# Kernel optimization log

Hardware: AMD Instinct MI355X
Metric: run time of the kernel (lower is better)

Reference implementation:

```python
import jax, jax.numpy as jnp
import numpy as np

ROUTING_ITER = 3
EPS = 1e-8


def squash(caps, axis=-1, eps=EPS):
    dot = jnp.sum(caps * caps, axis=axis, keepdims=True)
    scale = dot / (1.0 + dot) / jnp.sqrt(dot + eps)
    return scale * caps


def setup_inputs() -> dict:
    key = jax.random.key(0)
    k1, k2, k3 = jax.random.split(key, 3)
    B, I, O, D_in, D_out = 32, 1024, 64, 16, 32
    x = jax.random.normal(k1, (B, I, D_in), dtype=jnp.float32)
    W = jax.random.normal(k2, (1, I, O, D_out, D_in), dtype=jnp.float32) * 0.05
    b = jax.random.normal(k3, (1, 1, O, D_out), dtype=jnp.float32) * 0.05
    return {"x": x, "W": W, "b": b}


def reference(x, W, b):
    # u_hat[b,i,o,d] = sum_n W[0,i,o,d,n] * x[b,i,n]
    u_hat = jnp.einsum('iodn,bin->biod', W[0], x)  # [B, I, O, D_out]
    u_hat_det = jax.lax.stop_gradient(u_hat)
    B, I, O, _ = u_hat.shape
    b_ij = jnp.zeros((B, I, O, 1), dtype=x.dtype)
    v_j = None
    for it in range(ROUTING_ITER):
        c_ij = jax.nn.softmax(b_ij, axis=2)  # over output capsules
        if it == ROUTING_ITER - 1:
            s_j = jnp.sum(c_ij * u_hat, axis=1, keepdims=True) + b  # [B,1,O,D]
            v_j = squash(s_j, axis=-1)
        else:
            s_j = jnp.sum(c_ij * u_hat_det, axis=1, keepdims=True)
            v_j = squash(s_j, axis=-1)
            a_ij = jnp.sum(u_hat_det * v_j, axis=-1, keepdims=True)  # agreement
            b_ij = b_ij + a_ij
    return jnp.squeeze(v_j)  # [B, O, D_out]
```

## Files before the change

### kernel.cpp

```cpp
#include <hip/hip_runtime.h>
#include <hip/hip_bf16.h>
#include <stdint.h>

#define B_  32
#define I_  1024
#define O_  64
#define D_  32
#define N_  16
#define OD_ 2048

__device__ __forceinline__ uint32_t f2bf1(float f) {
  uint32_t u = __float_as_uint(f);
  return (u + 0x7fffu + ((u >> 16) & 1u)) >> 16;
}
__device__ __forceinline__ uint32_t pack2(float a, float b) {
  return f2bf1(a) | (f2bf1(b) << 16);
}
__device__ __forceinline__ void unpack8(uint4 r, float u[8]) {
  u[0] = __uint_as_float(r.x << 16);
  u[1] = __uint_as_float(r.x & 0xffff0000u);
  u[2] = __uint_as_float(r.y << 16);
  u[3] = __uint_as_float(r.y & 0xffff0000u);
  u[4] = __uint_as_float(r.z << 16);
  u[5] = __uint_as_float(r.z & 0xffff0000u);
  u[6] = __uint_as_float(r.w << 16);
  u[7] = __uint_as_float(r.w & 0xffff0000u);
}

__global__ __launch_bounds__(256) void k_einsum(const float* __restrict__ x,
                                                const float* __restrict__ W,
                                                uint4* __restrict__ uhat) {
  const int i = blockIdx.x;
  const int t = threadIdx.x;
  __shared__ float xs[B_ * N_];
  for (int e = t; e < B_ * N_; e += 256) {
    int bb = e >> 4, n = e & 15;
    xs[e] = x[(size_t)bb * (I_ * N_) + (size_t)i * N_ + n];
  }
  float w[8][16];
  const float* Wi = W + (size_t)i * (OD_ * N_) + (size_t)t * (8 * N_);
  #pragma unroll
  for (int k = 0; k < 8; ++k) {
    #pragma unroll
    for (int q = 0; q < 4; ++q) {
      float4 f = ((const float4*)(Wi + k * 16))[q];
      w[k][q * 4 + 0] = f.x; w[k][q * 4 + 1] = f.y;
      w[k][q * 4 + 2] = f.z; w[k][q * 4 + 3] = f.w;
    }
  }
  __syncthreads();
  for (int bb = 0; bb < B_; ++bb) {
    float xv[16];
    #pragma unroll
    for (int q = 0; q < 4; ++q) {
      float4 f = ((const float4*)(xs + bb * 16))[q];
      xv[q * 4 + 0] = f.x; xv[q * 4 + 1] = f.y;
      xv[q * 4 + 2] = f.z; xv[q * 4 + 3] = f.w;
    }
    float acc[8];
    #pragma unroll
    for (int k = 0; k < 8; ++k) {
      float a = 0.f;
      #pragma unroll
      for (int n = 0; n < 16; ++n) a = fmaf(w[k][n], xv[n], a);
      acc[k] = a;
    }
    uint4 outv = make_uint4(pack2(acc[0], acc[1]), pack2(acc[2], acc[3]),
                            pack2(acc[4], acc[5]), pack2(acc[6], acc[7]));
    uhat[(((size_t)bb * I_ + i) * OD_ + (size_t)t * 8) >> 3] = outv;
  }
}

__global__ __launch_bounds__(256) void k_sum0(const uint4* __restrict__ uhat,
                                              float* __restrict__ part) {
  const int b = blockIdx.x >> 5, chunk = blockIdx.x & 31;
  const int t = threadIdx.x;
  float acc[8] = {0.f, 0.f, 0.f, 0.f, 0.f, 0.f, 0.f, 0.f};
  for (int ii = 0; ii < 32; ++ii) {
    const int i = chunk * 32 + ii;
    uint4 r = uhat[(((size_t)b * I_ + i) * OD_ + (size_t)t * 8) >> 3];
    float u[8]; unpack8(r, u);
    #pragma unroll
    for (int j = 0; j < 8; ++j) acc[j] += u[j];
  }
  float* o = part + ((size_t)b * 32 + chunk) * OD_ + (size_t)t * 8;
  ((float4*)o)[0] = make_float4(acc[0], acc[1], acc[2], acc[3]);
  ((float4*)o)[1] = make_float4(acc[4], acc[5], acc[6], acc[7]);
}

__global__ __launch_bounds__(256) void k_squash(const float* __restrict__ part,
                                                const float* __restrict__ bias,
                                                float* __restrict__ vout,
                                                float scale, int addBias) {
  const int lane = threadIdx.x & 63;
  const int row = blockIdx.x * 4 + (threadIdx.x >> 6);
  const int b = row >> 6, o = row & 63;
  const int d = lane & 31;
  const float* p = part + (size_t)b * (32 * OD_) + (size_t)o * 32 + d;
  float s = 0.f;
  const int c0 = (lane >> 5) * 16;
  for (int c = c0; c < c0 + 16; ++c) s += p[(size_t)c * OD_];
  s += __shfl_xor(s, 32);
  s *= scale;
  if (addBias) s += bias[o * 32 + d];
  float dot = s * s;
  #pragma unroll
  for (int off = 1; off <= 16; off <<= 1) dot += __shfl_xor(dot, off);
  float sc = dot / (1.f + dot) / sqrtf(dot + 1e-8f);
  if (lane < 32) vout[(size_t)row * 32 + d] = s * sc;
}

__global__ __launch_bounds__(256) void k_route(const uint4* __restrict__ uhat,
                                               const float* __restrict__ vprev,
                                               float* __restrict__ bij,
                                               float* __restrict__ part,
                                               int secondIter) {
  const int b = blockIdx.x >> 5, chunk = blockIdx.x & 31;
  const int t = threadIdx.x;
  __shared__ float abuf[64];
  __shared__ float cbuf[64];
  float vreg[8];
  {
    const float4* vp = (const float4*)(vprev + (size_t)b * OD_ + (size_t)t * 8);
    float4 v0 = vp[0], v1 = vp[1];
    vreg[0] = v0.x; vreg[1] = v0.y; vreg[2] = v0.z; vreg[3] = v0.w;
    vreg[4] = v1.x; vreg[5] = v1.y; vreg[6] = v1.z; vreg[7] = v1.w;
  }
  float s_acc[8] = {0.f, 0.f, 0.f, 0.f, 0.f, 0.f, 0.f, 0.f};
  for (int ii = 0; ii < 32; ++ii) {
    const int i = chunk * 32 + ii;
    uint4 r = uhat[(((size_t)b * I_ + i) * OD_ + (size_t)t * 8) >> 3];
    float u[8]; unpack8(r, u);
    float p = 0.f;
    #pragma unroll
    for (int j = 0; j < 8; ++j) p = fmaf(u[j], vreg[j], p);
    p += __shfl_xor(p, 1);
    p += __shfl_xor(p, 2);
    if ((t & 3) == 0) abuf[t >> 2] = p;
    __syncthreads();
    if (t < 64) {
      float a = abuf[t];
      const size_t bidx = ((size_t)b * I_ + i) * 64 + t;
      float bn;
      if (secondIter) bn = bij[bidx] + a;
      else            { bn = a; bij[bidx] = bn; }
      float m = bn;
      #pragma unroll
      for (int off = 1; off <= 32; off <<= 1) m = fmaxf(m, __shfl_xor(m, off));
      float e = __expf(bn - m);
      float sm = e;
      #pragma unroll
      for (int off = 1; off <= 32; off <<= 1) sm += __shfl_xor(sm, off);
      cbuf[t] = e / sm;
    }
    __syncthreads();
    const float c = cbuf[t >> 2];
    #pragma unroll
    for (int j = 0; j < 8; ++j) s_acc[j] = fmaf(c, u[j], s_acc[j]);
  }
  float* o = part + ((size_t)b * 32 + chunk) * OD_ + (size_t)t * 8;
  ((float4*)o)[0] = make_float4(s_acc[0], s_acc[1], s_acc[2], s_acc[3]);
  ((float4*)o)[1] = make_float4(s_acc[4], s_acc[5], s_acc[6], s_acc[7]);
}

extern "C" void kernel_launch(void* const* d_in, const int* in_sizes, int n_in,
                              void* d_out, int out_size, void* d_ws, size_t ws_size,
                              hipStream_t stream) {
  const float* x    = (const float*)d_in[0];
  const float* W    = (const float*)d_in[1];
  const float* bias = (const float*)d_in[2];
  float* out = (float*)d_out;

  char* ws = (char*)d_ws;
  uint4* uhat = (uint4*)ws;
  float* bij  = (float*)(ws + 134217728ull);
  float* part = (float*)(ws + 134217728ull + 8388608ull);
  float* vbuf = (float*)(ws + 134217728ull + 16777216ull);

  k_einsum<<<dim3(I_), dim3(256), 0, stream>>>(x, W, uhat);
  k_sum0  <<<dim3(1024), dim3(256), 0, stream>>>(uhat, part);
  k_squash<<<dim3(512),  dim3(256), 0, stream>>>(part, bias, vbuf, 1.f / 64.f, 0);
  k_route <<<dim3(1024), dim3(256), 0, stream>>>(uhat, vbuf, bij, part, 0);
  k_squash<<<dim3(512),  dim3(256), 0, stream>>>(part, bias, vbuf, 1.f, 0);
  k_route <<<dim3(1024), dim3(256), 0, stream>>>(uhat, vbuf, bij, part, 1);
  k_squash<<<dim3(512),  dim3(256), 0, stream>>>(part, bias, out, 1.f, 1);
}
```

Measured before the change: 346.1 us.

## Batch routing softmax across 32 inputs and split einsum blocks in half

```diff
diff --git a/kernel.cpp b/kernel.cpp
--- a/kernel.cpp
+++ b/kernel.cpp
@@ -29,18 +29,20 @@
 
 __global__ __launch_bounds__(256) void k_einsum(const float* __restrict__ x,
                                                 const float* __restrict__ W,
-                                                uint4* __restrict__ uhat) {
-  const int i = blockIdx.x;
+                                                uint2* __restrict__ uhat) {
+  const int i = blockIdx.x >> 1;
+  const int half = blockIdx.x & 1;
   const int t = threadIdx.x;
+  const int od_base = half * 1024 + t * 4;
   __shared__ float xs[B_ * N_];
   for (int e = t; e < B_ * N_; e += 256) {
     int bb = e >> 4, n = e & 15;
     xs[e] = x[(size_t)bb * (I_ * N_) + (size_t)i * N_ + n];
   }
-  float w[8][16];
-  const float* Wi = W + (size_t)i * (OD_ * N_) + (size_t)t * (8 * N_);
+  float w[4][16];
+  const float* Wi = W + (size_t)i * (OD_ * N_) + (size_t)od_base * N_;
   #pragma unroll
-  for (int k = 0; k < 8; ++k) {
+  for (int k = 0; k < 4; ++k) {
     #pragma unroll
     for (int q = 0; q < 4; ++q) {
       float4 f = ((const float4*)(Wi + k * 16))[q];
@@ -57,17 +59,16 @@
       xv[q * 4 + 0] = f.x; xv[q * 4 + 1] = f.y;
       xv[q * 4 + 2] = f.z; xv[q * 4 + 3] = f.w;
     }
-    float acc[8];
-    #pragma unroll
-    for (int k = 0; k < 8; ++k) {
+    float acc[4];
+    #pragma unroll
+    for (int k = 0; k < 4; ++k) {
       float a = 0.f;
       #pragma unroll
       for (int n = 0; n < 16; ++n) a = fmaf(w[k][n], xv[n], a);
       acc[k] = a;
     }
-    uint4 outv = make_uint4(pack2(acc[0], acc[1]), pack2(acc[2], acc[3]),
-                            pack2(acc[4], acc[5]), pack2(acc[6], acc[7]));
-    uhat[(((size_t)bb * I_ + i) * OD_ + (size_t)t * 8) >> 3] = outv;
+    uhat[(((size_t)bb * I_ + i) * OD_ + od_base) >> 2] =
+        make_uint2(pack2(acc[0], acc[1]), pack2(acc[2], acc[3]));
   }
 }
 
@@ -110,6 +111,7 @@
   if (lane < 32) vout[(size_t)row * 32 + d] = s * sc;
 }
 
+#define PAD_ 65
 __global__ __launch_bounds__(256) void k_route(const uint4* __restrict__ uhat,
                                                const float* __restrict__ vprev,
                                                float* __restrict__ bij,
@@ -117,8 +119,8 @@
                                                int secondIter) {
   const int b = blockIdx.x >> 5, chunk = blockIdx.x & 31;
   const int t = threadIdx.x;
-  __shared__ float abuf[64];
-  __shared__ float cbuf[64];
+  __shared__ float abuf[32 * PAD_];
+  __shared__ float cbuf[32 * PAD_];
   float vreg[8];
   {
     const float4* vp = (const float4*)(vprev + (size_t)b * OD_ + (size_t)t * 8);
@@ -126,35 +128,64 @@
     vreg[0] = v0.x; vreg[1] = v0.y; vreg[2] = v0.z; vreg[3] = v0.w;
     vreg[4] = v1.x; vreg[5] = v1.y; vreg[6] = v1.z; vreg[7] = v1.w;
   }
-  float s_acc[8] = {0.f, 0.f, 0.f, 0.f, 0.f, 0.f, 0.f, 0.f};
+  const size_t ubase = (((size_t)b * I_ + (size_t)chunk * 32) * OD_ + (size_t)t * 8) >> 3;
   for (int ii = 0; ii < 32; ++ii) {
-    const int i = chunk * 32 + ii;
-    uint4 r = uhat[(((size_t)b * I_ + i) * OD_ + (size_t)t * 8) >> 3];
+    uint4 r = uhat[ubase + (size_t)ii * (OD_ / 8)];
     float u[8]; unpack8(r, u);
     float p = 0.f;
     #pragma unroll
     for (int j = 0; j < 8; ++j) p = fmaf(u[j], vreg[j], p);
     p += __shfl_xor(p, 1);
     p += __shfl_xor(p, 2);
-    if ((t & 3) == 0) abuf[t >> 2] = p;
-    __syncthreads();
-    if (t < 64) {
-      float a = abuf[t];
-      const size_t bidx = ((size_t)b * I_ + i) * 64 + t;
-      float bn;
-      if (secondIter) bn = bij[bidx] + a;
-      else            { bn = a; bij[bidx] = bn; }
-      float m = bn;
+    if ((t & 3) == 0) abuf[ii * PAD_ + (t >> 2)] = p;
+  }
+  __syncthreads();
+  {
+    const int ii = t >> 3;
+    const int ob = (t & 7) * 8;
+    const int i = chunk * 32 + ii;
+    float bn[8];
+    const size_t bidx = ((size_t)b * I_ + i) * 64 + ob;
+    if (secondIter) {
+      float4 b0 = ((const float4*)(bij + bidx))[0];
+      float4 b1 = ((const float4*)(bij + bidx))[1];
+      bn[0] = b0.x + abuf[ii * PAD_ + ob + 0];
+      bn[1] = b0.y + abuf[ii * PAD_ + ob + 1];
+      bn[2] = b0.z + abuf[ii * PAD_ + ob + 2];
+      bn[3] = b0.w + abuf[ii * PAD_ + ob + 3];
+      bn[4] = b1.x + abuf[ii * PAD_ + ob + 4];
+      bn[5] = b1.y + abuf[ii * PAD_ + ob + 5];
+      bn[6] = b1.z + abuf[ii * PAD_ + ob + 6];
+      bn[7] = b1.w + abuf[ii * PAD_ + ob + 7];
+    } else {
       #pragma unroll
-      for (int off = 1; off <= 32; off <<= 1) m = fmaxf(m, __shfl_xor(m, off));
-      float e = __expf(bn - m);
-      float sm = e;
-      #pragma unroll
-      for (int off = 1; off <= 32; off <<= 1) sm += __shfl_xor(sm, off);
-      cbuf[t] = e / sm;
-    }
-    __syncthreads();
-    const float c = cbuf[t >> 2];
+      for (int j = 0; j < 8; ++j) bn[j] = abuf[ii * PAD_ + ob + j];
+      ((float4*)(bij + bidx))[0] = make_float4(bn[0], bn[1], bn[2], bn[3]);
+      ((float4*)(bij + bidx))[1] = make_float4(bn[4], bn[5], bn[6], bn[7]);
+    }
+    float m = bn[0];
+    #pragma unroll
+    for (int j = 1; j < 8; ++j) m = fmaxf(m, bn[j]);
+    m = fmaxf(m, __shfl_xor(m, 1));
+    m = fmaxf(m, __shfl_xor(m, 2));
+    m = fmaxf(m, __shfl_xor(m, 4));
+    float e[8], sm = 0.f;
+    #pragma unroll
+    for (int j = 0; j < 8; ++j) { e[j] = __expf(bn[j] - m); sm += e[j]; }
+    sm += __shfl_xor(sm, 1);
+    sm += __shfl_xor(sm, 2);
+    sm += __shfl_xor(sm, 4);
+    float inv = 1.f / sm;
+    #pragma unroll
+    for (int j = 0; j < 8; ++j) cbuf[ii * PAD_ + ob + j] = e[j] * inv;
+  }
+  __syncthreads();
+  float s_acc[8] = {0.f, 0.f, 0.f, 0.f, 0.f, 0.f, 0.f, 0.f};
+  const int oq = t >> 2;
+  for (int ii = 0; ii < 32; ++ii) {
+    uint4 r = uhat[ubase + (size_t)ii * (OD_ / 8)];
+    float u[8]; unpack8(r, u);
+    const float c = cbuf[ii * PAD_ + oq];
     #pragma unroll
     for (int j = 0; j < 8; ++j) s_acc[j] = fmaf(c, u[j], s_acc[j]);
   }
@@ -172,16 +203,17 @@
   float* out = (float*)d_out;
 
   char* ws = (char*)d_ws;
-  uint4* uhat = (uint4*)ws;
+  uint2* uhat2 = (uint2*)ws;
+  uint4* uhat4 = (uint4*)ws;
   float* bij  = (float*)(ws + 134217728ull);
   float* part = (float*)(ws + 134217728ull + 8388608ull);
   float* vbuf = (float*)(ws + 134217728ull + 16777216ull);
 
-  k_einsum<<<dim3(I_), dim3(256), 0, stream>>>(x, W, uhat);
-  k_sum0  <<<dim3(1024), dim3(256), 0, stream>>>(uhat, part);
+  k_einsum<<<dim3(I_ * 2), dim3(256), 0, stream>>>(x, W, uhat2);
+  k_sum0  <<<dim3(1024), dim3(256), 0, stream>>>(uhat4, part);
   k_squash<<<dim3(512),  dim3(256), 0, stream>>>(part, bias, vbuf, 1.f / 64.f, 0);
-  k_route <<<dim3(1024), dim3(256), 0, stream>>>(uhat, vbuf, bij, part, 0);
+  k_route <<<dim3(1024), dim3(256), 0, stream>>>(uhat4, vbuf, bij, part, 0);
   k_squash<<<dim3(512),  dim3(256), 0, stream>>>(part, bias, vbuf, 1.f, 0);
-  k_route <<<dim3(1024), dim3(256), 0, stream>>>(uhat, vbuf, bij, part, 1);
+  k_route <<<dim3(1024), dim3(256), 0, stream>>>(uhat4, vbuf, bij, part, 1);
   k_squash<<<dim3(512),  dim3(256), 0, stream>>>(part, bias, out, 1.f, 1);
 }
```

Measured after the change: 336.5 us. 1.03x faster.
